# Kernel tuning notes

Measured on AMD Instinct MI355X. Metric: run time of the kernel, lower is better.

## Reference

```python
import jax, jax.numpy as jnp
import numpy as np

E = 8        # n_routed_experts
Z = 4        # zero_expert_num (identity experts)
K = 2        # moe_topk
SCALE = 2.5  # routed_scaling_factor
T, H, I = 8192, 1024, 512


def setup_inputs() -> dict:
    key = jax.random.key(0)
    k0, k1, k2, k3, k4 = jax.random.split(key, 5)
    return {
        "hidden_states": jax.random.normal(k0, (T, H), jnp.float32),
        "router_w": jax.random.normal(k1, (E + Z, H), jnp.float32) * 0.02,
        "correction_bias": jax.random.normal(k2, (E + Z,), jnp.float32) * 0.01,
        "w13": jax.random.normal(k3, (E, 2 * I, H), jnp.float32) * 0.02,
        "w2": jax.random.normal(k4, (E, H, I), jnp.float32) * 0.02,
    }


def reference(hidden_states, router_w, correction_bias, w13, w2):
    # ---- router (float32) ----
    logits = hidden_states.astype(jnp.float32) @ router_w.T          # [T, E+Z]
    scores = jax.nn.softmax(logits, axis=-1)
    # correction bias only affects expert *selection*, not the gate weights
    _, topk_idx = jax.lax.top_k(scores + correction_bias, K)          # [T, K]
    topk_w = jnp.take_along_axis(scores, topk_idx, axis=-1)          # renormalize=False

    # ---- zero experts (identity type): idx >= E contributes scale * x ----
    is_zero = topk_idx >= E                                           # [T, K]
    routed_w = jnp.where(is_zero, 0.0, topk_w)
    zero_scale = jnp.where(is_zero, topk_w, 0.0).sum(-1, keepdims=True)
    zero_result = zero_scale * hidden_states                          # [T, H]

    # ---- combine weights per routed expert: [T, E] ----
    tok = jnp.arange(hidden_states.shape[0])[:, None]
    safe_idx = jnp.clip(topk_idx, 0, E - 1)   # zero-expert slots carry weight 0
    combine = jnp.zeros((hidden_states.shape[0], E), scores.dtype)
    combine = combine.at[tok, safe_idx].add(routed_w)

    # ---- grouped expert GEMMs (SiLU gated MLP), combined densely ----
    h = jnp.einsum('th,eih->eti', hidden_states, w13)                 # [E, T, 2I]
    g, u = jnp.split(h, 2, axis=-1)
    act = jax.nn.silu(g) * u                                          # [E, T, I]
    eo = jnp.einsum('eti,ehi->eth', act, w2)                          # [E, T, H]
    routed = jnp.einsum('te,eth->th', combine, eo)                    # [T, H]

    return routed * SCALE + zero_result
```

## Files before the change

kernel.cpp:

```cpp
#include <hip/hip_runtime.h>
#include <hip/hip_bf16.h>
#include <math.h>

typedef __bf16 bf16_t;
typedef bf16_t bf16x8 __attribute__((ext_vector_type(8)));
typedef float f32x4 __attribute__((ext_vector_type(4)));

#define T_TOK 8192
#define HDIM  1024
#define IDIM  512
#define NEXP  8
#define NTOT  12
#define MAXROWS (2 * T_TOK + NEXP * 128)
#define MAX_MTILES (MAXROWS / 128)

__device__ __forceinline__ void gll16(const bf16_t* g, bf16_t* l) {
  __builtin_amdgcn_global_load_lds((__attribute__((address_space(1))) void*)g,
                                   (__attribute__((address_space(3))) void*)l,
                                   16, 0, 0);
}

__device__ __forceinline__ bf16x8 cvt8(float4 f0, float4 f1) {
  bf16x8 t;
  t[0] = (bf16_t)f0.x; t[1] = (bf16_t)f0.y; t[2] = (bf16_t)f0.z; t[3] = (bf16_t)f0.w;
  t[4] = (bf16_t)f1.x; t[5] = (bf16_t)f1.y; t[6] = (bf16_t)f1.z; t[7] = (bf16_t)f1.w;
  return t;
}

#define N1G (NEXP * 2 * IDIM * HDIM / 8)
#define N2G (NEXP * HDIM * IDIM / 8)
__global__ void cast_w_kernel(const float* __restrict__ w13, const float* __restrict__ w2,
                              bf16_t* __restrict__ w13b, bf16_t* __restrict__ w2b) {
  size_t gid = (size_t)blockIdx.x * blockDim.x + threadIdx.x;
  const float* src;
  bf16_t* dst;
  if (gid < N1G) { src = w13 + gid * 8; dst = w13b + gid * 8; }
  else { size_t g2 = gid - N1G; if (g2 >= N2G) return; src = w2 + g2 * 8; dst = w2b + g2 * 8; }
  float4 a = *(const float4*)src;
  float4 b = *(const float4*)(src + 4);
  *(bf16x8*)dst = cvt8(a, b);
}

__global__ void zero_counts_kernel(int* __restrict__ counts) {
  if (threadIdx.x < NEXP) counts[threadIdx.x] = 0;
}

__global__ void router_kernel(const float* __restrict__ x, const float* __restrict__ rw,
                              const float* __restrict__ bias,
                              int* __restrict__ tk_e, float* __restrict__ tk_w,
                              float* __restrict__ zscale, int* __restrict__ counts) {
  __shared__ int lc[NEXP];
  int tid = threadIdx.x;
  if (tid < NEXP) lc[tid] = 0;
  __syncthreads();
  int t = blockIdx.x * 4 + (tid >> 6);
  int l = tid & 63;
  const float4* xr = (const float4*)(x + (size_t)t * HDIM);
  float4 xv[4];
#pragma unroll
  for (int i = 0; i < 4; i++) xv[i] = xr[l + 64 * i];
  float part[NTOT];
#pragma unroll
  for (int e = 0; e < NTOT; e++) {
    const float4* wr = (const float4*)(rw + (size_t)e * HDIM);
    float s = 0.f;
#pragma unroll
    for (int i = 0; i < 4; i++) {
      float4 w = wr[l + 64 * i];
      s += xv[i].x * w.x + xv[i].y * w.y + xv[i].z * w.z + xv[i].w * w.w;
    }
    part[e] = s;
  }
#pragma unroll
  for (int off = 32; off > 0; off >>= 1)
#pragma unroll
    for (int e = 0; e < NTOT; e++) part[e] += __shfl_down(part[e], off);

  if (l == 0) {
    float mx = part[0];
#pragma unroll
    for (int e = 1; e < NTOT; e++) mx = fmaxf(mx, part[e]);
    float p[NTOT], den = 0.f;
#pragma unroll
    for (int e = 0; e < NTOT; e++) { p[e] = expf(part[e] - mx); den += p[e]; }
    float inv = 1.f / den;
#pragma unroll
    for (int e = 0; e < NTOT; e++) p[e] *= inv;
    float s0 = -1e30f, s1 = -1e30f; int i0 = 0, i1 = 0;
#pragma unroll
    for (int e = 0; e < NTOT; e++) {
      float v = p[e] + bias[e];
      if (v > s0) { s1 = s0; i1 = i0; s0 = v; i0 = e; }
      else if (v > s1) { s1 = v; i1 = e; }
    }
    float zs = 0.f;
    int idx[2] = { i0, i1 };
#pragma unroll
    for (int k = 0; k < 2; k++) {
      int e = idx[k];
      float w = p[e];
      if (e >= NEXP) { zs += w; tk_e[2 * t + k] = -1; tk_w[2 * t + k] = 0.f; }
      else { tk_e[2 * t + k] = e; tk_w[2 * t + k] = w; atomicAdd(&lc[e], 1); }
    }
    zscale[t] = zs;
  }
  __syncthreads();
  if (tid < NEXP && lc[tid]) atomicAdd(&counts[tid], lc[tid]);
}

__global__ void scan_kernel(const int* __restrict__ counts, int* __restrict__ cursor,
                            int* __restrict__ tile_e, int* __restrict__ tile_p0,
                            int* __restrict__ n_mtiles,
                            int* __restrict__ sel_tok, float* __restrict__ sel_w) {
  __shared__ int s_off[NEXP], s_cnt[NEXP];
  if (threadIdx.x == 0) {
    int run = 0, nt = 0;
    for (int e = 0; e < NEXP; e++) {
      s_off[e] = run; s_cnt[e] = counts[e];
      cursor[e] = run;
      int ntile = (s_cnt[e] + 127) / 128;
      for (int i = 0; i < ntile; i++) { tile_e[nt] = e; tile_p0[nt] = run + i * 128; nt++; }
      run += ntile * 128;
    }
    *n_mtiles = nt;
  }
  __syncthreads();
  for (int i = threadIdx.x; i < NEXP * 128; i += blockDim.x) {
    int e = i >> 7, idx = i & 127;
    int c = s_cnt[e];
    int padded = ((c + 127) / 128) * 128;
    int pos = c + idx;
    if (pos < padded) { sel_tok[s_off[e] + pos] = 0; sel_w[s_off[e] + pos] = 0.f; }
  }
}

__global__ void assign_kernel(const int* __restrict__ tk_e, const float* __restrict__ tk_w,
                              int* __restrict__ cursor, int* __restrict__ sel_tok,
                              float* __restrict__ sel_w, int* __restrict__ pos) {
  __shared__ int lc[NEXP], lbase[NEXP];
  int tid = threadIdx.x;
  if (tid < NEXP) lc[tid] = 0;
  __syncthreads();
  int t = blockIdx.x * blockDim.x + tid;
  int e0 = tk_e[2 * t], e1 = tk_e[2 * t + 1];
  int r0 = (e0 >= 0) ? atomicAdd(&lc[e0], 1) : -1;
  int r1 = (e1 >= 0) ? atomicAdd(&lc[e1], 1) : -1;
  __syncthreads();
  if (tid < NEXP) lbase[tid] = lc[tid] ? atomicAdd(&cursor[tid], lc[tid]) : 0;
  __syncthreads();
  int p0 = -1, p1 = -1;
  if (e0 >= 0) { p0 = lbase[e0] + r0; sel_tok[p0] = t; sel_w[p0] = 2.5f * tk_w[2 * t]; }
  if (e1 >= 0) { p1 = lbase[e1] + r1; sel_tok[p1] = t; sel_w[p1] = 2.5f * tk_w[2 * t + 1]; }
  pos[2 * t] = p0;
  pos[2 * t + 1] = p1;
}

__global__ void gather_out_kernel(const float* __restrict__ x, const float* __restrict__ zscale,
                                  const int* __restrict__ pos, bf16_t* __restrict__ xg,
                                  float* __restrict__ out) {
  size_t gid = (size_t)blockIdx.x * blockDim.x + threadIdx.x;
  size_t t = gid >> 7;
  int j = (int)(gid & 127) * 8;
  float zs = zscale[t];
  int p0 = pos[2 * t], p1 = pos[2 * t + 1];
  float4 a = *(const float4*)&x[t * HDIM + j];
  float4 b = *(const float4*)&x[t * HDIM + j + 4];
  *(float4*)&out[t * HDIM + j] = make_float4(zs * a.x, zs * a.y, zs * a.z, zs * a.w);
  *(float4*)&out[t * HDIM + j + 4] = make_float4(zs * b.x, zs * b.y, zs * b.z, zs * b.w);
  bf16x8 o = cvt8(a, b);
  if (p0 >= 0) *(bf16x8*)&xg[(size_t)p0 * HDIM + j] = o;
  if (p1 >= 0) *(bf16x8*)&xg[(size_t)p1 * HDIM + j] = o;
}


__global__ __launch_bounds__(256) void gemm1_kernel(
    const bf16_t* __restrict__ xg, const bf16_t* __restrict__ w13b,
    const int* __restrict__ tile_e, const int* __restrict__ tile_p0,
    const int* __restrict__ n_mtiles, bf16_t* __restrict__ actb) {
  const int yb = blockIdx.x & 7;
  const int ti = blockIdx.x >> 3;
  if (ti >= *n_mtiles) return;
  const int e = tile_e[ti];
  const int p0 = tile_p0[ti];
  const int g0 = yb * 64;

  __shared__ alignas(16) bf16_t As[128 * 32];
  __shared__ alignas(16) bf16_t Bs[128 * 32];
  const int tid = threadIdx.x;
  const int w = tid >> 6, l = tid & 63;
  const int wr = w >> 1, wc = w & 1;
  const int quad = l >> 4, c16 = l & 15;

  const int sr = w * 32 + (l >> 2);
  const int sr1 = sr + 16;
  const int sc0 = ((l & 3) ^ ((sr >> 1) & 3)) * 8;
  const int sc1 = ((l & 3) ^ ((sr1 >> 1) & 3)) * 8;
  const bf16_t* Ag0 = xg + (size_t)(p0 + sr) * HDIM + sc0;
  const bf16_t* Ag1 = xg + (size_t)(p0 + sr1) * HDIM + sc1;
  int col0 = g0 + (sr >> 6) * 32 + (((sr >> 4) & 1) * 16) + (sr & 15) + (((sr >> 5) & 1) ? IDIM : 0);
  int col1 = g0 + (sr1 >> 6) * 32 + (((sr1 >> 4) & 1) * 16) + (sr1 & 15) + (((sr1 >> 5) & 1) ? IDIM : 0);
  const bf16_t* w13e = w13b + (size_t)e * (2 * IDIM) * HDIM;
  const bf16_t* Bg0 = w13e + (size_t)col0 * HDIM + sc0;
  const bf16_t* Bg1 = w13e + (size_t)col1 * HDIM + sc1;
  bf16_t* Al0 = &As[(w * 32) * 32];
  bf16_t* Bl0 = &Bs[(w * 32) * 32];

  int aoff[4], boff[4];
#pragma unroll
  for (int mt = 0; mt < 4; mt++) {
    int r = wr * 64 + mt * 16 + c16;
    aoff[mt] = r * 32 + ((quad ^ ((r >> 1) & 3)) * 8);
  }
#pragma unroll
  for (int nt = 0; nt < 4; nt++) {
    int r = wc * 64 + nt * 16 + c16;
    boff[nt] = r * 32 + ((quad ^ ((r >> 1) & 3)) * 8);
  }

  f32x4 acc[4][4];
#pragma unroll
  for (int i = 0; i < 4; i++)
#pragma unroll
    for (int j = 0; j < 4; j++) acc[i][j] = (f32x4){0.f, 0.f, 0.f, 0.f};

  for (int k0 = 0; k0 < HDIM; k0 += 32) {
    gll16(Ag0 + k0, Al0);
    gll16(Ag1 + k0, Al0 + 16 * 32);
    gll16(Bg0 + k0, Bl0);
    gll16(Bg1 + k0, Bl0 + 16 * 32);
    __syncthreads();
    bf16x8 af[4], bfv[4];
#pragma unroll
    for (int mt = 0; mt < 4; mt++) af[mt] = *(const bf16x8*)&As[aoff[mt]];
#pragma unroll
    for (int nt = 0; nt < 4; nt++) bfv[nt] = *(const bf16x8*)&Bs[boff[nt]];
#pragma unroll
    for (int mt = 0; mt < 4; mt++)
#pragma unroll
      for (int nt = 0; nt < 4; nt++)
        acc[mt][nt] = __builtin_amdgcn_mfma_f32_16x16x32_bf16(af[mt], bfv[nt], acc[mt][nt], 0, 0, 0);
    __syncthreads();
  }

#pragma unroll
  for (int mt = 0; mt < 4; mt++) {
    int rowb = p0 + wr * 64 + mt * 16 + quad * 4;
#pragma unroll
    for (int nt = 0; nt < 2; nt++) {
      int col = g0 + wc * 32 + nt * 16 + c16;
#pragma unroll
      for (int r = 0; r < 4; r++) {
        float g = acc[mt][nt][r];
        float u = acc[mt][nt + 2][r];
        actb[(size_t)(rowb + r) * IDIM + col] = (bf16_t)(g / (1.f + expf(-g)) * u);
      }
    }
  }
}

__global__ __launch_bounds__(256) void gemm2_kernel(
    const bf16_t* __restrict__ actb, const bf16_t* __restrict__ w2b,
    const float* __restrict__ sel_w, const int* __restrict__ sel_tok,
    const int* __restrict__ tile_e, const int* __restrict__ tile_p0,
    const int* __restrict__ n_mtiles, float* __restrict__ out) {
  const int yb = blockIdx.x & 7;
  const int ti = blockIdx.x >> 3;
  if (ti >= *n_mtiles) return;
  const int e = tile_e[ti];
  const int p0 = tile_p0[ti];
  const int n0 = yb * 128;

  __shared__ alignas(16) bf16_t As[128 * 32];
  __shared__ alignas(16) bf16_t Bs[128 * 32];
  const int tid = threadIdx.x;
  const int w = tid >> 6, l = tid & 63;
  const int wr = w >> 1, wc = w & 1;
  const int quad = l >> 4, c16 = l & 15;

  const int sr = w * 32 + (l >> 2);
  const int sr1 = sr + 16;
  const int sc0 = ((l & 3) ^ ((sr >> 1) & 3)) * 8;
  const int sc1 = ((l & 3) ^ ((sr1 >> 1) & 3)) * 8;
  const bf16_t* Ag0 = actb + (size_t)(p0 + sr) * IDIM + sc0;
  const bf16_t* Ag1 = actb + (size_t)(p0 + sr1) * IDIM + sc1;
  const bf16_t* w2e = w2b + (size_t)e * HDIM * IDIM;
  const bf16_t* Bg0 = w2e + (size_t)(n0 + sr) * IDIM + sc0;
  const bf16_t* Bg1 = w2e + (size_t)(n0 + sr1) * IDIM + sc1;
  bf16_t* Al0 = &As[(w * 32) * 32];
  bf16_t* Bl0 = &Bs[(w * 32) * 32];

  int aoff[4], boff[4];
#pragma unroll
  for (int mt = 0; mt < 4; mt++) {
    int r = wr * 64 + mt * 16 + c16;
    aoff[mt] = r * 32 + ((quad ^ ((r >> 1) & 3)) * 8);
  }
#pragma unroll
  for (int nt = 0; nt < 4; nt++) {
    int r = wc * 64 + nt * 16 + c16;
    boff[nt] = r * 32 + ((quad ^ ((r >> 1) & 3)) * 8);
  }

  f32x4 acc[4][4];
#pragma unroll
  for (int i = 0; i < 4; i++)
#pragma unroll
    for (int j = 0; j < 4; j++) acc[i][j] = (f32x4){0.f, 0.f, 0.f, 0.f};

  for (int k0 = 0; k0 < IDIM; k0 += 32) {
    gll16(Ag0 + k0, Al0);
    gll16(Ag1 + k0, Al0 + 16 * 32);
    gll16(Bg0 + k0, Bl0);
    gll16(Bg1 + k0, Bl0 + 16 * 32);
    __syncthreads();
    bf16x8 af[4], bfv[4];
#pragma unroll
    for (int mt = 0; mt < 4; mt++) af[mt] = *(const bf16x8*)&As[aoff[mt]];
#pragma unroll
    for (int nt = 0; nt < 4; nt++) bfv[nt] = *(const bf16x8*)&Bs[boff[nt]];
#pragma unroll
    for (int mt = 0; mt < 4; mt++)
#pragma unroll
      for (int nt = 0; nt < 4; nt++)
        acc[mt][nt] = __builtin_amdgcn_mfma_f32_16x16x32_bf16(af[mt], bfv[nt], acc[mt][nt], 0, 0, 0);
    __syncthreads();
  }

#pragma unroll
  for (int mt = 0; mt < 4; mt++) {
    int rowb = p0 + wr * 64 + mt * 16 + quad * 4;
#pragma unroll
    for (int r = 0; r < 4; r++) {
      int p = rowb + r;
      float cw = sel_w[p];
      if (cw == 0.f) continue;
      size_t obase = (size_t)sel_tok[p] * HDIM;
#pragma unroll
      for (int nt = 0; nt < 4; nt++) {
        int col = n0 + wc * 64 + nt * 16 + c16;
        atomicAdd(&out[obase + col], cw * acc[mt][nt][r]);
      }
    }
  }
}

extern "C" void kernel_launch(void* const* d_in, const int* in_sizes, int n_in,
                              void* d_out, int out_size, void* d_ws, size_t ws_size,
                              hipStream_t stream) {
  const float* x    = (const float*)d_in[0];
  const float* rw   = (const float*)d_in[1];
  const float* bias = (const float*)d_in[2];
  const float* w13  = (const float*)d_in[3];
  const float* w2   = (const float*)d_in[4];
  float* out = (float*)d_out;

  char* ws = (char*)d_ws;
  bf16_t* w13b = (bf16_t*)ws;  ws += (size_t)NEXP * 2 * IDIM * HDIM * 2;
  bf16_t* w2b  = (bf16_t*)ws;  ws += (size_t)NEXP * HDIM * IDIM * 2;
  bf16_t* xg   = (bf16_t*)ws;  ws += (size_t)MAXROWS * HDIM * 2;
  bf16_t* actb = (bf16_t*)ws;  ws += (size_t)MAXROWS * IDIM * 2;
  int*   tk_e    = (int*)ws;   ws += (size_t)T_TOK * 2 * 4;
  float* tk_w    = (float*)ws; ws += (size_t)T_TOK * 2 * 4;
  float* zscale  = (float*)ws; ws += (size_t)T_TOK * 4;
  int*   pos     = (int*)ws;   ws += (size_t)T_TOK * 2 * 4;
  int*   sel_tok = (int*)ws;   ws += (size_t)MAXROWS * 4;
  float* sel_w   = (float*)ws; ws += (size_t)MAXROWS * 4;
  int*   counts  = (int*)ws;   ws += NEXP * 4;
  int*   cursor  = (int*)ws;   ws += NEXP * 4;
  int*   tile_e  = (int*)ws;   ws += MAX_MTILES * 4;
  int*   tile_p0 = (int*)ws;   ws += MAX_MTILES * 4;
  int*   n_mtiles = (int*)ws;  ws += 4;

  zero_counts_kernel<<<1, 64, 0, stream>>>(counts);
  cast_w_kernel<<<(N1G + N2G + 255) / 256, 256, 0, stream>>>(w13, w2, w13b, w2b);
  router_kernel<<<T_TOK / 4, 256, 0, stream>>>(x, rw, bias, tk_e, tk_w, zscale, counts);
  scan_kernel<<<1, 256, 0, stream>>>(counts, cursor, tile_e, tile_p0, n_mtiles, sel_tok, sel_w);
  assign_kernel<<<T_TOK / 256, 256, 0, stream>>>(tk_e, tk_w, cursor, sel_tok, sel_w, pos);
  gather_out_kernel<<<(size_t)T_TOK * (HDIM / 8) / 256, 256, 0, stream>>>(
      x, zscale, pos, xg, out);

  gemm1_kernel<<<MAX_MTILES * 8, 256, 0, stream>>>(
      xg, w13b, tile_e, tile_p0, n_mtiles, actb);
  gemm2_kernel<<<MAX_MTILES * 8, 256, 0, stream>>>(
      actb, w2b, sel_w, sel_tok, tile_e, tile_p0, n_mtiles, out);
}
```

Before: 264.7 us.

## Double GEMM K-tile depth and replace atomic scatter with per-slot buffer plus combine

Both grouped GEMMs now stage a 64-wide K slice per barrier pair instead of 32, using a new 8-chunk XOR swizzle. This halves the number of syncs and load issues per output tile. The second GEMM no longer atomically adds into the token-ordered output. It writes weighted bf16 results per sorted slot, and a new combine kernel sums the two slots plus the zero-expert term per token. This removes float atomics at the cost of an extra bf16 intermediate buffer, one more pass over the output, and bf16 rounding of the expert outputs before the sum.

New measurement: 259.2 us. 1.02x faster.

```diff
diff --git a/kernel.cpp b/kernel.cpp
--- a/kernel.cpp
+++ b/kernel.cpp
@@ -13,6 +13,7 @@
 #define NTOT  12
 #define MAXROWS (2 * T_TOK + NEXP * 128)
 #define MAX_MTILES (MAXROWS / 128)
+#define BK 64
 
 __device__ __forceinline__ void gll16(const bf16_t* g, bf16_t* l) {
   __builtin_amdgcn_global_load_lds((__attribute__((address_space(1))) void*)g,
@@ -155,23 +156,24 @@
   pos[2 * t + 1] = p1;
 }
 
-__global__ void gather_out_kernel(const float* __restrict__ x, const float* __restrict__ zscale,
-                                  const int* __restrict__ pos, bf16_t* __restrict__ xg,
-                                  float* __restrict__ out) {
+__global__ void gather_kernel(const float* __restrict__ x, const int* __restrict__ pos,
+                              bf16_t* __restrict__ xg) {
   size_t gid = (size_t)blockIdx.x * blockDim.x + threadIdx.x;
   size_t t = gid >> 7;
   int j = (int)(gid & 127) * 8;
-  float zs = zscale[t];
   int p0 = pos[2 * t], p1 = pos[2 * t + 1];
+  if (p0 < 0 && p1 < 0) return;
   float4 a = *(const float4*)&x[t * HDIM + j];
   float4 b = *(const float4*)&x[t * HDIM + j + 4];
-  *(float4*)&out[t * HDIM + j] = make_float4(zs * a.x, zs * a.y, zs * a.z, zs * a.w);
-  *(float4*)&out[t * HDIM + j + 4] = make_float4(zs * b.x, zs * b.y, zs * b.z, zs * b.w);
   bf16x8 o = cvt8(a, b);
   if (p0 >= 0) *(bf16x8*)&xg[(size_t)p0 * HDIM + j] = o;
   if (p1 >= 0) *(bf16x8*)&xg[(size_t)p1 * HDIM + j] = o;
 }
 
+
+__device__ __forceinline__ int colmap1(int r, int g0) {
+  return g0 + ((r >> 6) & 1) * 32 + (((r >> 4) & 1) * 16) + (r & 15) + (((r >> 5) & 1) ? IDIM : 0);
+}
 
 __global__ __launch_bounds__(256) void gemm1_kernel(
     const bf16_t* __restrict__ xg, const bf16_t* __restrict__ w13b,
@@ -184,37 +186,42 @@
   const int p0 = tile_p0[ti];
   const int g0 = yb * 64;
 
-  __shared__ alignas(16) bf16_t As[128 * 32];
-  __shared__ alignas(16) bf16_t Bs[128 * 32];
+  __shared__ alignas(16) bf16_t As[128 * BK];
+  __shared__ alignas(16) bf16_t Bs[128 * BK];
   const int tid = threadIdx.x;
   const int w = tid >> 6, l = tid & 63;
   const int wr = w >> 1, wc = w & 1;
   const int quad = l >> 4, c16 = l & 15;
-
-  const int sr = w * 32 + (l >> 2);
-  const int sr1 = sr + 16;
-  const int sc0 = ((l & 3) ^ ((sr >> 1) & 3)) * 8;
-  const int sc1 = ((l & 3) ^ ((sr1 >> 1) & 3)) * 8;
-  const bf16_t* Ag0 = xg + (size_t)(p0 + sr) * HDIM + sc0;
-  const bf16_t* Ag1 = xg + (size_t)(p0 + sr1) * HDIM + sc1;
-  int col0 = g0 + (sr >> 6) * 32 + (((sr >> 4) & 1) * 16) + (sr & 15) + (((sr >> 5) & 1) ? IDIM : 0);
-  int col1 = g0 + (sr1 >> 6) * 32 + (((sr1 >> 4) & 1) * 16) + (sr1 & 15) + (((sr1 >> 5) & 1) ? IDIM : 0);
+  const int lrow = l >> 3, lch = l & 7;
+
   const bf16_t* w13e = w13b + (size_t)e * (2 * IDIM) * HDIM;
-  const bf16_t* Bg0 = w13e + (size_t)col0 * HDIM + sc0;
-  const bf16_t* Bg1 = w13e + (size_t)col1 * HDIM + sc1;
-  bf16_t* Al0 = &As[(w * 32) * 32];
-  bf16_t* Bl0 = &Bs[(w * 32) * 32];
-
-  int aoff[4], boff[4];
-#pragma unroll
-  for (int mt = 0; mt < 4; mt++) {
-    int r = wr * 64 + mt * 16 + c16;
-    aoff[mt] = r * 32 + ((quad ^ ((r >> 1) & 3)) * 8);
-  }
-#pragma unroll
-  for (int nt = 0; nt < 4; nt++) {
-    int r = wc * 64 + nt * 16 + c16;
-    boff[nt] = r * 32 + ((quad ^ ((r >> 1) & 3)) * 8);
+  const bf16_t* Asrc[4];
+  const bf16_t* Bsrc[4];
+  bf16_t* Adst[4];
+  bf16_t* Bdst[4];
+#pragma unroll
+  for (int c = 0; c < 4; c++) {
+    int r = w * 32 + c * 8 + lrow;
+    int sch = (lch ^ (r & 7)) * 8;
+    Asrc[c] = xg + (size_t)(p0 + r) * HDIM + sch;
+    Bsrc[c] = w13e + (size_t)colmap1(r, g0) * HDIM + sch;
+    Adst[c] = &As[(w * 32 + c * 8) * BK];
+    Bdst[c] = &Bs[(w * 32 + c * 8) * BK];
+  }
+
+  int aoff[2][4], boff[2][4];
+#pragma unroll
+  for (int h = 0; h < 2; h++) {
+#pragma unroll
+    for (int mt = 0; mt < 4; mt++) {
+      int r = wr * 64 + mt * 16 + c16;
+      aoff[h][mt] = r * BK + (((h * 4 + quad) ^ (r & 7)) * 8);
+    }
+#pragma unroll
+    for (int nt = 0; nt < 4; nt++) {
+      int r = wc * 64 + nt * 16 + c16;
+      boff[h][nt] = r * BK + (((h * 4 + quad) ^ (r & 7)) * 8);
+    }
   }
 
   f32x4 acc[4][4];
@@ -223,22 +230,26 @@
 #pragma unroll
     for (int j = 0; j < 4; j++) acc[i][j] = (f32x4){0.f, 0.f, 0.f, 0.f};
 
-  for (int k0 = 0; k0 < HDIM; k0 += 32) {
-    gll16(Ag0 + k0, Al0);
-    gll16(Ag1 + k0, Al0 + 16 * 32);
-    gll16(Bg0 + k0, Bl0);
-    gll16(Bg1 + k0, Bl0 + 16 * 32);
+  for (int k0 = 0; k0 < HDIM; k0 += BK) {
+#pragma unroll
+    for (int c = 0; c < 4; c++) {
+      gll16(Asrc[c] + k0, Adst[c]);
+      gll16(Bsrc[c] + k0, Bdst[c]);
+    }
     __syncthreads();
-    bf16x8 af[4], bfv[4];
-#pragma unroll
-    for (int mt = 0; mt < 4; mt++) af[mt] = *(const bf16x8*)&As[aoff[mt]];
-#pragma unroll
-    for (int nt = 0; nt < 4; nt++) bfv[nt] = *(const bf16x8*)&Bs[boff[nt]];
-#pragma unroll
-    for (int mt = 0; mt < 4; mt++)
-#pragma unroll
-      for (int nt = 0; nt < 4; nt++)
-        acc[mt][nt] = __builtin_amdgcn_mfma_f32_16x16x32_bf16(af[mt], bfv[nt], acc[mt][nt], 0, 0, 0);
+#pragma unroll
+    for (int h = 0; h < 2; h++) {
+      bf16x8 af[4], bfv[4];
+#pragma unroll
+      for (int mt = 0; mt < 4; mt++) af[mt] = *(const bf16x8*)&As[aoff[h][mt]];
+#pragma unroll
+      for (int nt = 0; nt < 4; nt++) bfv[nt] = *(const bf16x8*)&Bs[boff[h][nt]];
+#pragma unroll
+      for (int mt = 0; mt < 4; mt++)
+#pragma unroll
+        for (int nt = 0; nt < 4; nt++)
+          acc[mt][nt] = __builtin_amdgcn_mfma_f32_16x16x32_bf16(af[mt], bfv[nt], acc[mt][nt], 0, 0, 0);
+    }
     __syncthreads();
   }
 
@@ -260,9 +271,9 @@
 
 __global__ __launch_bounds__(256) void gemm2_kernel(
     const bf16_t* __restrict__ actb, const bf16_t* __restrict__ w2b,
-    const float* __restrict__ sel_w, const int* __restrict__ sel_tok,
-    const int* __restrict__ tile_e, const int* __restrict__ tile_p0,
-    const int* __restrict__ n_mtiles, float* __restrict__ out) {
+    const float* __restrict__ sel_w, const int* __restrict__ tile_e,
+    const int* __restrict__ tile_p0, const int* __restrict__ n_mtiles,
+    bf16_t* __restrict__ eob) {
   const int yb = blockIdx.x & 7;
   const int ti = blockIdx.x >> 3;
   if (ti >= *n_mtiles) return;
@@ -270,35 +281,42 @@
   const int p0 = tile_p0[ti];
   const int n0 = yb * 128;
 
-  __shared__ alignas(16) bf16_t As[128 * 32];
-  __shared__ alignas(16) bf16_t Bs[128 * 32];
+  __shared__ alignas(16) bf16_t As[128 * BK];
+  __shared__ alignas(16) bf16_t Bs[128 * BK];
   const int tid = threadIdx.x;
   const int w = tid >> 6, l = tid & 63;
   const int wr = w >> 1, wc = w & 1;
   const int quad = l >> 4, c16 = l & 15;
-
-  const int sr = w * 32 + (l >> 2);
-  const int sr1 = sr + 16;
-  const int sc0 = ((l & 3) ^ ((sr >> 1) & 3)) * 8;
-  const int sc1 = ((l & 3) ^ ((sr1 >> 1) & 3)) * 8;
-  const bf16_t* Ag0 = actb + (size_t)(p0 + sr) * IDIM + sc0;
-  const bf16_t* Ag1 = actb + (size_t)(p0 + sr1) * IDIM + sc1;
+  const int lrow = l >> 3, lch = l & 7;
+
   const bf16_t* w2e = w2b + (size_t)e * HDIM * IDIM;
-  const bf16_t* Bg0 = w2e + (size_t)(n0 + sr) * IDIM + sc0;
-  const bf16_t* Bg1 = w2e + (size_t)(n0 + sr1) * IDIM + sc1;
-  bf16_t* Al0 = &As[(w * 32) * 32];
-  bf16_t* Bl0 = &Bs[(w * 32) * 32];
-
-  int aoff[4], boff[4];
-#pragma unroll
-  for (int mt = 0; mt < 4; mt++) {
-    int r = wr * 64 + mt * 16 + c16;
-    aoff[mt] = r * 32 + ((quad ^ ((r >> 1) & 3)) * 8);
-  }
-#pragma unroll
-  for (int nt = 0; nt < 4; nt++) {
-    int r = wc * 64 + nt * 16 + c16;
-    boff[nt] = r * 32 + ((quad ^ ((r >> 1) & 3)) * 8);
+  const bf16_t* Asrc[4];
+  const bf16_t* Bsrc[4];
+  bf16_t* Adst[4];
+  bf16_t* Bdst[4];
+#pragma unroll
+  for (int c = 0; c < 4; c++) {
+    int r = w * 32 + c * 8 + lrow;
+    int sch = (lch ^ (r & 7)) * 8;
+    Asrc[c] = actb + (size_t)(p0 + r) * IDIM + sch;
+    Bsrc[c] = w2e + (size_t)(n0 + r) * IDIM + sch;
+    Adst[c] = &As[(w * 32 + c * 8) * BK];
+    Bdst[c] = &Bs[(w * 32 + c * 8) * BK];
+  }
+
+  int aoff[2][4], boff[2][4];
+#pragma unroll
+  for (int h = 0; h < 2; h++) {
+#pragma unroll
+    for (int mt = 0; mt < 4; mt++) {
+      int r = wr * 64 + mt * 16 + c16;
+      aoff[h][mt] = r * BK + (((h * 4 + quad) ^ (r & 7)) * 8);
+    }
+#pragma unroll
+    for (int nt = 0; nt < 4; nt++) {
+      int r = wc * 64 + nt * 16 + c16;
+      boff[h][nt] = r * BK + (((h * 4 + quad) ^ (r & 7)) * 8);
+    }
   }
 
   f32x4 acc[4][4];
@@ -307,22 +325,26 @@
 #pragma unroll
     for (int j = 0; j < 4; j++) acc[i][j] = (f32x4){0.f, 0.f, 0.f, 0.f};
 
-  for (int k0 = 0; k0 < IDIM; k0 += 32) {
-    gll16(Ag0 + k0, Al0);
-    gll16(Ag1 + k0, Al0 + 16 * 32);
-    gll16(Bg0 + k0, Bl0);
-    gll16(Bg1 + k0, Bl0 + 16 * 32);
+  for (int k0 = 0; k0 < IDIM; k0 += BK) {
+#pragma unroll
+    for (int c = 0; c < 4; c++) {
+      gll16(Asrc[c] + k0, Adst[c]);
+      gll16(Bsrc[c] + k0, Bdst[c]);
+    }
     __syncthreads();
-    bf16x8 af[4], bfv[4];
-#pragma unroll
-    for (int mt = 0; mt < 4; mt++) af[mt] = *(const bf16x8*)&As[aoff[mt]];
-#pragma unroll
-    for (int nt = 0; nt < 4; nt++) bfv[nt] = *(const bf16x8*)&Bs[boff[nt]];
-#pragma unroll
-    for (int mt = 0; mt < 4; mt++)
-#pragma unroll
-      for (int nt = 0; nt < 4; nt++)
-        acc[mt][nt] = __builtin_amdgcn_mfma_f32_16x16x32_bf16(af[mt], bfv[nt], acc[mt][nt], 0, 0, 0);
+#pragma unroll
+    for (int h = 0; h < 2; h++) {
+      bf16x8 af[4], bfv[4];
+#pragma unroll
+      for (int mt = 0; mt < 4; mt++) af[mt] = *(const bf16x8*)&As[aoff[h][mt]];
+#pragma unroll
+      for (int nt = 0; nt < 4; nt++) bfv[nt] = *(const bf16x8*)&Bs[boff[h][nt]];
+#pragma unroll
+      for (int mt = 0; mt < 4; mt++)
+#pragma unroll
+        for (int nt = 0; nt < 4; nt++)
+          acc[mt][nt] = __builtin_amdgcn_mfma_f32_16x16x32_bf16(af[mt], bfv[nt], acc[mt][nt], 0, 0, 0);
+    }
     __syncthreads();
   }
 
@@ -334,14 +356,40 @@
       int p = rowb + r;
       float cw = sel_w[p];
       if (cw == 0.f) continue;
-      size_t obase = (size_t)sel_tok[p] * HDIM;
+      size_t obase = (size_t)p * HDIM;
 #pragma unroll
       for (int nt = 0; nt < 4; nt++) {
         int col = n0 + wc * 64 + nt * 16 + c16;
-        atomicAdd(&out[obase + col], cw * acc[mt][nt][r]);
+        eob[obase + col] = (bf16_t)(cw * acc[mt][nt][r]);
       }
     }
   }
+}
+
+__global__ void combine_kernel(const float* __restrict__ x, const float* __restrict__ zscale,
+                               const int* __restrict__ pos, const bf16_t* __restrict__ eob,
+                               float* __restrict__ out) {
+  size_t gid = (size_t)blockIdx.x * blockDim.x + threadIdx.x;
+  size_t t = gid >> 7;
+  size_t j = (gid & 127) << 3;
+  float zs = zscale[t];
+  int p0 = pos[2 * t], p1 = pos[2 * t + 1];
+  float4 a = *(const float4*)&x[t * HDIM + j];
+  float4 b = *(const float4*)&x[t * HDIM + j + 4];
+  float o[8] = { zs * a.x, zs * a.y, zs * a.z, zs * a.w,
+                 zs * b.x, zs * b.y, zs * b.z, zs * b.w };
+  if (p0 >= 0) {
+    bf16x8 v = *(const bf16x8*)&eob[(size_t)p0 * HDIM + j];
+#pragma unroll
+    for (int k = 0; k < 8; k++) o[k] += (float)v[k];
+  }
+  if (p1 >= 0) {
+    bf16x8 v = *(const bf16x8*)&eob[(size_t)p1 * HDIM + j];
+#pragma unroll
+    for (int k = 0; k < 8; k++) o[k] += (float)v[k];
+  }
+  *(float4*)&out[t * HDIM + j] = make_float4(o[0], o[1], o[2], o[3]);
+  *(float4*)&out[t * HDIM + j + 4] = make_float4(o[4], o[5], o[6], o[7]);
 }
 
 extern "C" void kernel_launch(void* const* d_in, const int* in_sizes, int n_in,
@@ -359,6 +407,7 @@
   bf16_t* w2b  = (bf16_t*)ws;  ws += (size_t)NEXP * HDIM * IDIM * 2;
   bf16_t* xg   = (bf16_t*)ws;  ws += (size_t)MAXROWS * HDIM * 2;
   bf16_t* actb = (bf16_t*)ws;  ws += (size_t)MAXROWS * IDIM * 2;
+  bf16_t* eob  = (bf16_t*)ws;  ws += (size_t)MAXROWS * HDIM * 2;
   int*   tk_e    = (int*)ws;   ws += (size_t)T_TOK * 2 * 4;
   float* tk_w    = (float*)ws; ws += (size_t)T_TOK * 2 * 4;
   float* zscale  = (float*)ws; ws += (size_t)T_TOK * 4;
@@ -376,11 +425,13 @@
   router_kernel<<<T_TOK / 4, 256, 0, stream>>>(x, rw, bias, tk_e, tk_w, zscale, counts);
   scan_kernel<<<1, 256, 0, stream>>>(counts, cursor, tile_e, tile_p0, n_mtiles, sel_tok, sel_w);
   assign_kernel<<<T_TOK / 256, 256, 0, stream>>>(tk_e, tk_w, cursor, sel_tok, sel_w, pos);
-  gather_out_kernel<<<(size_t)T_TOK * (HDIM / 8) / 256, 256, 0, stream>>>(
-      x, zscale, pos, xg, out);
+  gather_kernel<<<(size_t)T_TOK * (HDIM / 8) / 256, 256, 0, stream>>>(x, pos, xg);
 
   gemm1_kernel<<<MAX_MTILES * 8, 256, 0, stream>>>(
       xg, w13b, tile_e, tile_p0, n_mtiles, actb);
   gemm2_kernel<<<MAX_MTILES * 8, 256, 0, stream>>>(
-      actb, w2b, sel_w, sel_tok, tile_e, tile_p0, n_mtiles, out);
-}
+      actb, w2b, sel_w, tile_e, tile_p0, n_mtiles, eob);
+
+  combine_kernel<<<(size_t)T_TOK * HDIM / 8 / 256, 256, 0, stream>>>(
+      x, zscale, pos, eob, out);
+}
```

## Replace gemm2 atomic scatter with bf16 per-slot output and separate combine kernel

Applied to the files above, without the earlier changes.

gemm2 now writes weighted expert outputs as bf16 into a per-slot buffer instead of doing fp32 atomicAdd into the output, and a new combine kernel sums the zero-expert term and up to two slot rows per token. The aim is to remove the cost of contended global atomics and the separate initial write of out. The gather kernel skips tokens that have no routed slots, and zeroing of counts moves into the weight-cast kernel, dropping one launch. In exchange it adds an extra MAXROWS x H bf16 round trip plus one more launch, and rounding the expert outputs to bf16 reduces precision.

Result: faster. 247.2 us (-6.6%).

```diff
diff --git a/kernel.cpp b/kernel.cpp
--- a/kernel.cpp
+++ b/kernel.cpp
@@ -30,7 +30,9 @@
 #define N1G (NEXP * 2 * IDIM * HDIM / 8)
 #define N2G (NEXP * HDIM * IDIM / 8)
 __global__ void cast_w_kernel(const float* __restrict__ w13, const float* __restrict__ w2,
-                              bf16_t* __restrict__ w13b, bf16_t* __restrict__ w2b) {
+                              bf16_t* __restrict__ w13b, bf16_t* __restrict__ w2b,
+                              int* __restrict__ counts) {
+  if (blockIdx.x == 0 && threadIdx.x < NEXP) counts[threadIdx.x] = 0;
   size_t gid = (size_t)blockIdx.x * blockDim.x + threadIdx.x;
   const float* src;
   bf16_t* dst;
@@ -39,10 +41,6 @@
   float4 a = *(const float4*)src;
   float4 b = *(const float4*)(src + 4);
   *(bf16x8*)dst = cvt8(a, b);
-}
-
-__global__ void zero_counts_kernel(int* __restrict__ counts) {
-  if (threadIdx.x < NEXP) counts[threadIdx.x] = 0;
 }
 
 __global__ void router_kernel(const float* __restrict__ x, const float* __restrict__ rw,
@@ -155,18 +153,15 @@
   pos[2 * t + 1] = p1;
 }
 
-__global__ void gather_out_kernel(const float* __restrict__ x, const float* __restrict__ zscale,
-                                  const int* __restrict__ pos, bf16_t* __restrict__ xg,
-                                  float* __restrict__ out) {
+__global__ void gather_kernel(const float* __restrict__ x, const int* __restrict__ pos,
+                              bf16_t* __restrict__ xg) {
   size_t gid = (size_t)blockIdx.x * blockDim.x + threadIdx.x;
   size_t t = gid >> 7;
   int j = (int)(gid & 127) * 8;
-  float zs = zscale[t];
   int p0 = pos[2 * t], p1 = pos[2 * t + 1];
+  if (p0 < 0 && p1 < 0) return;
   float4 a = *(const float4*)&x[t * HDIM + j];
   float4 b = *(const float4*)&x[t * HDIM + j + 4];
-  *(float4*)&out[t * HDIM + j] = make_float4(zs * a.x, zs * a.y, zs * a.z, zs * a.w);
-  *(float4*)&out[t * HDIM + j + 4] = make_float4(zs * b.x, zs * b.y, zs * b.z, zs * b.w);
   bf16x8 o = cvt8(a, b);
   if (p0 >= 0) *(bf16x8*)&xg[(size_t)p0 * HDIM + j] = o;
   if (p1 >= 0) *(bf16x8*)&xg[(size_t)p1 * HDIM + j] = o;
@@ -260,9 +255,9 @@
 
 __global__ __launch_bounds__(256) void gemm2_kernel(
     const bf16_t* __restrict__ actb, const bf16_t* __restrict__ w2b,
-    const float* __restrict__ sel_w, const int* __restrict__ sel_tok,
-    const int* __restrict__ tile_e, const int* __restrict__ tile_p0,
-    const int* __restrict__ n_mtiles, float* __restrict__ out) {
+    const float* __restrict__ sel_w, const int* __restrict__ tile_e,
+    const int* __restrict__ tile_p0, const int* __restrict__ n_mtiles,
+    bf16_t* __restrict__ eob) {
   const int yb = blockIdx.x & 7;
   const int ti = blockIdx.x >> 3;
   if (ti >= *n_mtiles) return;
@@ -334,14 +329,40 @@
       int p = rowb + r;
       float cw = sel_w[p];
       if (cw == 0.f) continue;
-      size_t obase = (size_t)sel_tok[p] * HDIM;
+      size_t obase = (size_t)p * HDIM;
 #pragma unroll
       for (int nt = 0; nt < 4; nt++) {
         int col = n0 + wc * 64 + nt * 16 + c16;
-        atomicAdd(&out[obase + col], cw * acc[mt][nt][r]);
+        eob[obase + col] = (bf16_t)(cw * acc[mt][nt][r]);
       }
     }
   }
+}
+
+__global__ void combine_kernel(const float* __restrict__ x, const float* __restrict__ zscale,
+                               const int* __restrict__ pos, const bf16_t* __restrict__ eob,
+                               float* __restrict__ out) {
+  size_t gid = (size_t)blockIdx.x * blockDim.x + threadIdx.x;
+  size_t t = gid >> 7;
+  size_t j = (gid & 127) << 3;
+  float zs = zscale[t];
+  int p0 = pos[2 * t], p1 = pos[2 * t + 1];
+  float4 a = *(const float4*)&x[t * HDIM + j];
+  float4 b = *(const float4*)&x[t * HDIM + j + 4];
+  float o[8] = { zs * a.x, zs * a.y, zs * a.z, zs * a.w,
+                 zs * b.x, zs * b.y, zs * b.z, zs * b.w };
+  if (p0 >= 0) {
+    bf16x8 v = *(const bf16x8*)&eob[(size_t)p0 * HDIM + j];
+#pragma unroll
+    for (int k = 0; k < 8; k++) o[k] += (float)v[k];
+  }
+  if (p1 >= 0) {
+    bf16x8 v = *(const bf16x8*)&eob[(size_t)p1 * HDIM + j];
+#pragma unroll
+    for (int k = 0; k < 8; k++) o[k] += (float)v[k];
+  }
+  *(float4*)&out[t * HDIM + j] = make_float4(o[0], o[1], o[2], o[3]);
+  *(float4*)&out[t * HDIM + j + 4] = make_float4(o[4], o[5], o[6], o[7]);
 }
 
 extern "C" void kernel_launch(void* const* d_in, const int* in_sizes, int n_in,
@@ -359,6 +380,7 @@
   bf16_t* w2b  = (bf16_t*)ws;  ws += (size_t)NEXP * HDIM * IDIM * 2;
   bf16_t* xg   = (bf16_t*)ws;  ws += (size_t)MAXROWS * HDIM * 2;
   bf16_t* actb = (bf16_t*)ws;  ws += (size_t)MAXROWS * IDIM * 2;
+  bf16_t* eob  = (bf16_t*)ws;  ws += (size_t)MAXROWS * HDIM * 2;
   int*   tk_e    = (int*)ws;   ws += (size_t)T_TOK * 2 * 4;
   float* tk_w    = (float*)ws; ws += (size_t)T_TOK * 2 * 4;
   float* zscale  = (float*)ws; ws += (size_t)T_TOK * 4;
@@ -371,16 +393,17 @@
   int*   tile_p0 = (int*)ws;   ws += MAX_MTILES * 4;
   int*   n_mtiles = (int*)ws;  ws += 4;
 
-  zero_counts_kernel<<<1, 64, 0, stream>>>(counts);
-  cast_w_kernel<<<(N1G + N2G + 255) / 256, 256, 0, stream>>>(w13, w2, w13b, w2b);
+  cast_w_kernel<<<(N1G + N2G + 255) / 256, 256, 0, stream>>>(w13, w2, w13b, w2b, counts);
   router_kernel<<<T_TOK / 4, 256, 0, stream>>>(x, rw, bias, tk_e, tk_w, zscale, counts);
   scan_kernel<<<1, 256, 0, stream>>>(counts, cursor, tile_e, tile_p0, n_mtiles, sel_tok, sel_w);
   assign_kernel<<<T_TOK / 256, 256, 0, stream>>>(tk_e, tk_w, cursor, sel_tok, sel_w, pos);
-  gather_out_kernel<<<(size_t)T_TOK * (HDIM / 8) / 256, 256, 0, stream>>>(
-      x, zscale, pos, xg, out);
+  gather_kernel<<<(size_t)T_TOK * (HDIM / 8) / 256, 256, 0, stream>>>(x, pos, xg);
 
   gemm1_kernel<<<MAX_MTILES * 8, 256, 0, stream>>>(
       xg, w13b, tile_e, tile_p0, n_mtiles, actb);
   gemm2_kernel<<<MAX_MTILES * 8, 256, 0, stream>>>(
-      actb, w2b, sel_w, sel_tok, tile_e, tile_p0, n_mtiles, out);
-}
+      actb, w2b, sel_w, tile_e, tile_p0, n_mtiles, eob);
+
+  combine_kernel<<<(size_t)T_TOK * HDIM / 8 / 256, 256, 0, stream>>>(
+      x, zscale, pos, eob, out);
+}
```
